# Optimization experiments

Hardware: AMD Instinct MI355X
Metric: run time of the kernel (lower is better)

## Reference

```python
import jax, jax.numpy as jnp
import numpy as np

NUM_USERS = 100000
NUM_ITEMS = 50000
N = NUM_USERS + NUM_ITEMS
EMBED_DIM = 64
NUM_LAYERS = 3
NNZ = 4800000


def setup_inputs() -> dict:
    key = jax.random.key(0)
    k1, k2, k3, k4, k5 = jax.random.split(key, 5)
    user_emb = jax.random.normal(k1, (NUM_USERS, EMBED_DIM), dtype=jnp.float32)
    item_emb = jax.random.normal(k2, (NUM_ITEMS, EMBED_DIM), dtype=jnp.float32)
    edge_src = jax.random.randint(k3, (NNZ,), 0, N, dtype=jnp.int32)
    edge_dst = jax.random.randint(k4, (NNZ,), 0, N, dtype=jnp.int32)
    edge_val = jax.random.uniform(k5, (NNZ,), dtype=jnp.float32)
    return {"user_emb": user_emb, "item_emb": item_emb,
            "edge_src": edge_src, "edge_dst": edge_dst, "edge_val": edge_val}


def _spmm(edge_src, edge_dst, edge_val, x):
    # y[src] += val * x[dst]   (COO SpMM, fixed sparsity pattern)
    msgs = edge_val[:, None] * x[edge_dst]          # [nnz, D]
    return jax.ops.segment_sum(msgs, edge_src, num_segments=N)


def reference(user_emb, item_emb, edge_src, edge_dst, edge_val):
    ego = jnp.concatenate([user_emb, item_emb], axis=0)  # [N, D]
    acc = ego  # running sum for layer-mean pooling (avoids stacking all layers)
    for _ in range(NUM_LAYERS):
        ego = _spmm(edge_src, edge_dst, edge_val, ego)
        acc = acc + ego
    out = acc / jnp.float32(NUM_LAYERS + 1)  # mean over (num_layers+1) layer embeddings
    user_final = out[:NUM_USERS]
    item_final = out[NUM_USERS:]
    return (user_final, item_final)
```

## Files before the change

### kernel.cpp

```cpp
#include <hip/hip_runtime.h>
#include <hip/hip_fp16.h>

#define NUM_USERS 100000
#define NUM_ITEMS 50000
#define NTOT (NUM_USERS + NUM_ITEMS)
#define EMBED_DIM 64
#define NNZ_E 4800000
#define NUM_LAYERS 3

#define RPB 128
#define NBUCK ((NTOT + RPB - 1) / RPB)
#define BCAP 4672
#define NSUPER 37
#define SCAP 134144
#define EPB1 4096
#define EPB2 4096
#define DMASK 0x3FFFF
#define NBIN 19
#define NKEY (RPB * NBIN)
#define NKEYP 2560

__global__ void __launch_bounds__(256)
k_init(const float* __restrict__ ue, const float* __restrict__ ie,
       __half* __restrict__ b0) {
    const long long total2 = (long long)NTOT * EMBED_DIM / 2;
    const long long u2 = (long long)NUM_USERS * EMBED_DIM / 2;
    const float2* ue2 = (const float2*)ue;
    const float2* ie2 = (const float2*)ie;
    __half2* b02 = (__half2*)b0;
    for (long long i = (long long)blockIdx.x * blockDim.x + threadIdx.x;
         i < total2; i += (long long)gridDim.x * blockDim.x) {
        float2 v = (i < u2) ? ue2[i] : ie2[i - u2];
        b02[i] = __floats2half2_rn(v.x, v.y);
    }
}

__global__ void __launch_bounds__(256)
k_super(const int* __restrict__ src, const int* __restrict__ dst,
        const float* __restrict__ val, int* __restrict__ cursorS,
        int2* __restrict__ outS) {
    __shared__ int h[NSUPER];
    __shared__ int base[NSUPER];
    __shared__ int srcbuf[EPB1];
    int t = threadIdx.x;
    if (t < NSUPER) h[t] = 0;
    __syncthreads();
    long long e0 = (long long)blockIdx.x * EPB1;
    int n = (int)(((long long)NNZ_E - e0) < EPB1 ? (NNZ_E - e0) : EPB1);
    for (int i = t; i < n; i += 256) {
        int s = __builtin_nontemporal_load(&src[e0 + i]);
        srcbuf[i] = s;
        atomicAdd(&h[s >> 12], 1);
    }
    __syncthreads();
    if (t < NSUPER) {
        int c = h[t];
        base[t] = (c > 0) ? atomicAdd(&cursorS[t], c) : 0;
        h[t] = 0;
    }
    __syncthreads();
    for (int i = t; i < n; i += 256) {
        int s = srcbuf[i];
        int d = __builtin_nontemporal_load(&dst[e0 + i]);
        float v = __builtin_nontemporal_load(&val[e0 + i]);
        int sb = s >> 12;
        int off = base[sb] + atomicAdd(&h[sb], 1);
        outS[(long long)sb * SCAP + off] =
            make_int2(d | ((s & 4095) << 18), __float_as_int(v));
    }
}

__global__ void __launch_bounds__(256)
k_bin(const int2* __restrict__ superA, const int* __restrict__ cursorS,
      int* __restrict__ cursorB, int2* __restrict__ outB) {
    __shared__ int h[32];
    __shared__ int base32[32];
    int s = blockIdx.y;
    int cnt = cursorS[s];
    int beg = blockIdx.x * EPB2;
    if (beg >= cnt) return;
    int n = (cnt - beg < EPB2) ? (cnt - beg) : EPB2;
    int t = threadIdx.x;
    const long long* in8 = (const long long*)(superA + (long long)s * SCAP + beg);
    if (t < 32) h[t] = 0;
    __syncthreads();
    for (int i = t; i < n; i += 256) {
        long long raw = __builtin_nontemporal_load(&in8[i]);
        int row12 = ((int)raw >> 18) & 4095;
        atomicAdd(&h[row12 >> 7], 1);
    }
    __syncthreads();
    if (t < 32) {
        int c = h[t];
        base32[t] = (c > 0) ? atomicAdd(&cursorB[s * 32 + t], c) : 0;
        h[t] = 0;
    }
    __syncthreads();
    for (int i = t; i < n; i += 256) {
        long long raw = __builtin_nontemporal_load(&in8[i]);
        int ex = (int)raw;
        int row12 = (ex >> 18) & 4095;
        int bl = row12 >> 7;
        int off = base32[bl] + atomicAdd(&h[bl], 1);
        outB[(long long)(s * 32 + bl) * BCAP + off] =
            make_int2((ex & DMASK) | ((row12 & 127) << 18), (int)(raw >> 32));
    }
}

__global__ void __launch_bounds__(512)
k_sortip(int2* __restrict__ buf, const int* __restrict__ cursor,
         int2* __restrict__ rp) {
    __shared__ long long stage[BCAP];
    __shared__ int h[NKEYP];
    __shared__ int part[512];
    int b = blockIdx.x;
    int t = threadIdx.x;
    int cnt = cursor[b];
    long long gb = (long long)b * BCAP;
    long long* g8 = (long long*)buf + gb;
    for (int i = t; i < NKEYP; i += 512) h[i] = 0;
    __syncthreads();
    for (int i = t; i < cnt; i += 512) {
        long long raw = __builtin_nontemporal_load(&g8[i]);
        stage[i] = raw;
        int ex = (int)raw;
        int key = ((ex >> 18) & 127) * NBIN + ((ex & DMASK) >> 13);
        atomicAdd(&h[key], 1);
    }
    __syncthreads();
    int base = t * 5;
    int l0 = h[base], l1 = h[base + 1], l2 = h[base + 2], l3 = h[base + 3],
        l4 = h[base + 4];
    int s = l0 + l1 + l2 + l3 + l4;
    part[t] = s;
    __syncthreads();
    for (int off = 1; off < 512; off <<= 1) {
        int x = (t >= off) ? part[t - off] : 0;
        __syncthreads();
        part[t] += x;
        __syncthreads();
    }
    int run = part[t] - s;
    h[base] = run;     run += l0;
    h[base + 1] = run; run += l1;
    h[base + 2] = run; run += l2;
    h[base + 3] = run; run += l3;
    h[base + 4] = run;
    __syncthreads();
    if (t < RPB) {
        int beg = h[t * NBIN];
        int end = h[(t + 1) * NBIN];
        int row = b * RPB + t;
        if (row < NTOT)
            rp[row] = make_int2((int)(gb + beg), (int)(gb + end));
    }
    __syncthreads();
    for (int i = t; i < cnt; i += 512) {
        long long raw = stage[i];
        int ex = (int)raw;
        int key = ((ex >> 18) & 127) * NBIN + ((ex & DMASK) >> 13);
        int slot = atomicAdd(&h[key], 1);
        g8[slot] = raw;
    }
}

__device__ __forceinline__ void unpack4(float2 p, float& x0, float& x1,
                                        float& x2, float& x3) {
    __half2 h01 = *(const __half2*)&p.x;
    __half2 h23 = *(const __half2*)&p.y;
    float2 f01 = __half22float2(h01);
    float2 f23 = __half22float2(h23);
    x0 = f01.x; x1 = f01.y; x2 = f23.x; x3 = f23.y;
}

template <int U>
__device__ __forceinline__ void gg(const int2* __restrict__ edges, int j, int grp,
                                   int l16, const float2* __restrict__ xq,
                                   float& a0, float& a1, float& a2, float& a3) {
    int2 e[U];
    float2 xv[U];
#pragma unroll
    for (int k = 0; k < U; ++k) e[k] = edges[j + grp * U + k];
#pragma unroll
    for (int k = 0; k < U; ++k)
        xv[k] = xq[(long long)(e[k].x & DMASK) * 16 + l16];
#pragma unroll
    for (int k = 0; k < U; ++k) {
        float w = __int_as_float(e[k].y);
        float x0, x1, x2, x3;
        unpack4(xv[k], x0, x1, x2, x3);
        a0 = fmaf(w, x0, a0);
        a1 = fmaf(w, x1, a1);
        a2 = fmaf(w, x2, a2);
        a3 = fmaf(w, x3, a3);
    }
}

template <bool LAST>
__global__ void __launch_bounds__(256)
k_spmm_csr(const int2* __restrict__ edges, const int2* __restrict__ rp,
           const __half* __restrict__ x, __half* __restrict__ nxt,
           const __half* __restrict__ eb0, const __half* __restrict__ eb1,
           float* __restrict__ out) {
    int row = blockIdx.x * 4 + (threadIdx.x >> 6);
    int lane = threadIdx.x & 63;
    if (row >= NTOT) return;
    int2 be = rp[row];
    int beg = be.x;
    int end = be.y;
    int grp = lane >> 4;
    int l16 = lane & 15;
    const float2* xq = (const float2*)x;
    float a0 = 0.f, a1 = 0.f, a2 = 0.f, a3 = 0.f;
    int j = beg;
    for (; j + 32 <= end; j += 32) gg<8>(edges, j, grp, l16, xq, a0, a1, a2, a3);
    if (j + 16 <= end) { gg<4>(edges, j, grp, l16, xq, a0, a1, a2, a3); j += 16; }
    if (j + 8 <= end)  { gg<2>(edges, j, grp, l16, xq, a0, a1, a2, a3); j += 8; }
    for (int t2 = j + grp; t2 < end; t2 += 4) {
        int2 e = edges[t2];
        float w = __int_as_float(e.y);
        float x0, x1, x2, x3;
        unpack4(xq[(long long)(e.x & DMASK) * 16 + l16], x0, x1, x2, x3);
        a0 = fmaf(w, x0, a0);
        a1 = fmaf(w, x1, a1);
        a2 = fmaf(w, x2, a2);
        a3 = fmaf(w, x3, a3);
    }
    a0 += __shfl_xor(a0, 16); a1 += __shfl_xor(a1, 16);
    a2 += __shfl_xor(a2, 16); a3 += __shfl_xor(a3, 16);
    a0 += __shfl_xor(a0, 32); a1 += __shfl_xor(a1, 32);
    a2 += __shfl_xor(a2, 32); a3 += __shfl_xor(a3, 32);
    if (grp == 0) {
        if (!LAST) {
            union { __half2 h[2]; float2 f; } u;
            u.h[0] = __floats2half2_rn(a0, a1);
            u.h[1] = __floats2half2_rn(a2, a3);
            ((float2*)nxt)[(long long)row * 16 + l16] = u.f;
        } else {
            float v0, v1, v2, v3, w0, w1, w2, w3, z0, z1, z2, z3;
            unpack4(((const float2*)eb0)[(long long)row * 16 + l16], v0, v1, v2, v3);
            unpack4(((const float2*)eb1)[(long long)row * 16 + l16], w0, w1, w2, w3);
            unpack4(xq[(long long)row * 16 + l16], z0, z1, z2, z3);
            const float s = 1.0f / (NUM_LAYERS + 1);
            float4 r;
            r.x = (v0 + w0 + z0 + a0) * s;
            r.y = (v1 + w1 + z1 + a1) * s;
            r.z = (v2 + w2 + z2 + a2) * s;
            r.w = (v3 + w3 + z3 + a3) * s;
            ((float4*)out)[(long long)row * 16 + l16] = r;
        }
    }
}

extern "C" void kernel_launch(void* const* d_in, const int* in_sizes, int n_in,
                              void* d_out, int out_size, void* d_ws, size_t ws_size,
                              hipStream_t stream) {
    const float* user_emb = (const float*)d_in[0];
    const float* item_emb = (const float*)d_in[1];
    const int* edge_src   = (const int*)d_in[2];
    const int* edge_dst   = (const int*)d_in[3];
    const float* edge_val = (const float*)d_in[4];
    float* out = (float*)d_out;

    auto al = [](size_t x) { return (x + 255) & ~(size_t)255; };
    const size_t halfMat   = (size_t)NTOT * EMBED_DIM * sizeof(__half);
    const size_t buckBytes = al((size_t)NBUCK * BCAP * sizeof(int2));
    const size_t rpBytes   = al(((size_t)NTOT + 8) * sizeof(int2));

    char* p = (char*)d_ws;
    __half* b0 = (__half*)p;
    __half* b1 = (__half*)(p + halfMat);
    __half* b2 = (__half*)(p + 2 * halfMat);
    int2* superA = (int2*)d_ws;
    p += 3 * halfMat;
    int2* bucketedB = (int2*)p;          p += buckBytes;
    int2* rp = (int2*)p;                 p += rpBytes;
    int* cursorS = (int*)p;
    int* cursorB = cursorS + 64;

    hipMemsetAsync(cursorS, 0, 8192, stream);

    hipLaunchKernelGGL(k_super, dim3((NNZ_E + EPB1 - 1) / EPB1), dim3(256), 0,
                       stream, edge_src, edge_dst, edge_val, cursorS, superA);
    hipLaunchKernelGGL(k_bin, dim3((SCAP + EPB2 - 1) / EPB2, NSUPER), dim3(256),
                       0, stream, superA, cursorS, cursorB, bucketedB);
    hipLaunchKernelGGL(k_sortip, dim3(NBUCK), dim3(512), 0, stream,
                       bucketedB, cursorB, rp);
    hipLaunchKernelGGL(k_init, dim3(2048), dim3(256), 0, stream,
                       user_emb, item_emb, b0);

    const int spmmBlocks = (NTOT + 3) / 4;
    hipLaunchKernelGGL((k_spmm_csr<false>), dim3(spmmBlocks), dim3(256), 0,
                       stream, bucketedB, rp, b0, b1,
                       (const __half*)nullptr, (const __half*)nullptr, out);
    hipLaunchKernelGGL((k_spmm_csr<false>), dim3(spmmBlocks), dim3(256), 0,
                       stream, bucketedB, rp, b1, b2,
                       (const __half*)nullptr, (const __half*)nullptr, out);
    hipLaunchKernelGGL((k_spmm_csr<true>), dim3(spmmBlocks), dim3(256), 0,
                       stream, bucketedB, rp, b2, (__half*)nullptr,
                       b0, b1, out);
}
```

Before: 411.7 us.

## Replace per-row CSR SpMM with column-binned segmented SpMM over buckets

The sort kernel now keys edges by row and by one of 10 coarse column bins, and stores a per-row table of bin offsets instead of a single begin/end pair. The new SpMM kernel gives each 32-lane group 8 consecutive rows and walks the column bins in order, so all groups in a block gather from the same slice of the embedding matrix at the same time. The aim is better L2 reuse of the gathered half-precision rows. In exchange it gives up the old unrolled multi-edge gathers, leaving a short, serial per-row loop with little memory-level parallelism and fewer, larger blocks.

```diff
diff --git a/kernel.cpp b/kernel.cpp
--- a/kernel.cpp
+++ b/kernel.cpp
@@ -16,9 +16,9 @@
 #define EPB1 4096
 #define EPB2 4096
 #define DMASK 0x3FFFF
-#define NBIN 19
+#define NBIN 10
 #define NKEY (RPB * NBIN)
-#define NKEYP 2560
+#define RPS 16
 
 __global__ void __launch_bounds__(256)
 k_init(const float* __restrict__ ue, const float* __restrict__ ie,
@@ -109,145 +109,121 @@
 
 __global__ void __launch_bounds__(512)
 k_sortip(int2* __restrict__ buf, const int* __restrict__ cursor,
-         int2* __restrict__ rp) {
+         int* __restrict__ rp16) {
     __shared__ long long stage[BCAP];
-    __shared__ int h[NKEYP];
-    __shared__ int part[512];
+    __shared__ int h[NKEY];
+    __shared__ int part[256];
     int b = blockIdx.x;
     int t = threadIdx.x;
     int cnt = cursor[b];
     long long gb = (long long)b * BCAP;
     long long* g8 = (long long*)buf + gb;
-    for (int i = t; i < NKEYP; i += 512) h[i] = 0;
+    for (int i = t; i < NKEY; i += 512) h[i] = 0;
     __syncthreads();
     for (int i = t; i < cnt; i += 512) {
         long long raw = __builtin_nontemporal_load(&g8[i]);
         stage[i] = raw;
         int ex = (int)raw;
-        int key = ((ex >> 18) & 127) * NBIN + ((ex & DMASK) >> 13);
+        int key = ((ex >> 18) & 127) * NBIN + ((ex & DMASK) >> 14);
         atomicAdd(&h[key], 1);
     }
     __syncthreads();
+    int l0 = 0, l1 = 0, l2 = 0, l3 = 0, l4 = 0, s = 0;
     int base = t * 5;
-    int l0 = h[base], l1 = h[base + 1], l2 = h[base + 2], l3 = h[base + 3],
-        l4 = h[base + 4];
-    int s = l0 + l1 + l2 + l3 + l4;
-    part[t] = s;
-    __syncthreads();
-    for (int off = 1; off < 512; off <<= 1) {
-        int x = (t >= off) ? part[t - off] : 0;
+    if (t < 256) {
+        l0 = h[base]; l1 = h[base + 1]; l2 = h[base + 2];
+        l3 = h[base + 3]; l4 = h[base + 4];
+        s = l0 + l1 + l2 + l3 + l4;
+        part[t] = s;
+    }
+    __syncthreads();
+    for (int off = 1; off < 256; off <<= 1) {
+        int x = 0;
+        if (t < 256 && t >= off) x = part[t - off];
         __syncthreads();
-        part[t] += x;
+        if (t < 256) part[t] += x;
         __syncthreads();
     }
-    int run = part[t] - s;
-    h[base] = run;     run += l0;
-    h[base + 1] = run; run += l1;
-    h[base + 2] = run; run += l2;
-    h[base + 3] = run; run += l3;
-    h[base + 4] = run;
+    if (t < 256) {
+        int run = part[t] - s;
+        h[base] = run;     run += l0;
+        h[base + 1] = run; run += l1;
+        h[base + 2] = run; run += l2;
+        h[base + 3] = run; run += l3;
+        h[base + 4] = run;
+    }
     __syncthreads();
     if (t < RPB) {
-        int beg = h[t * NBIN];
-        int end = h[(t + 1) * NBIN];
         int row = b * RPB + t;
-        if (row < NTOT)
-            rp[row] = make_int2((int)(gb + beg), (int)(gb + end));
+        int gbi = (int)gb;
+#pragma unroll
+        for (int q = 0; q < NBIN; ++q)
+            rp16[row * RPS + q] = gbi + h[t * NBIN + q];
+        int end = (t == RPB - 1) ? cnt : h[(t + 1) * NBIN];
+        rp16[row * RPS + NBIN] = gbi + end;
     }
     __syncthreads();
     for (int i = t; i < cnt; i += 512) {
         long long raw = stage[i];
         int ex = (int)raw;
-        int key = ((ex >> 18) & 127) * NBIN + ((ex & DMASK) >> 13);
+        int key = ((ex >> 18) & 127) * NBIN + ((ex & DMASK) >> 14);
         int slot = atomicAdd(&h[key], 1);
         g8[slot] = raw;
     }
 }
 
-__device__ __forceinline__ void unpack4(float2 p, float& x0, float& x1,
-                                        float& x2, float& x3) {
-    __half2 h01 = *(const __half2*)&p.x;
-    __half2 h23 = *(const __half2*)&p.y;
-    float2 f01 = __half22float2(h01);
-    float2 f23 = __half22float2(h23);
-    x0 = f01.x; x1 = f01.y; x2 = f23.x; x3 = f23.y;
-}
-
-template <int U>
-__device__ __forceinline__ void gg(const int2* __restrict__ edges, int j, int grp,
-                                   int l16, const float2* __restrict__ xq,
-                                   float& a0, float& a1, float& a2, float& a3) {
-    int2 e[U];
-    float2 xv[U];
-#pragma unroll
-    for (int k = 0; k < U; ++k) e[k] = edges[j + grp * U + k];
-#pragma unroll
-    for (int k = 0; k < U; ++k)
-        xv[k] = xq[(long long)(e[k].x & DMASK) * 16 + l16];
-#pragma unroll
-    for (int k = 0; k < U; ++k) {
-        float w = __int_as_float(e[k].y);
-        float x0, x1, x2, x3;
-        unpack4(xv[k], x0, x1, x2, x3);
-        a0 = fmaf(w, x0, a0);
-        a1 = fmaf(w, x1, a1);
-        a2 = fmaf(w, x2, a2);
-        a3 = fmaf(w, x3, a3);
-    }
-}
-
 template <bool LAST>
-__global__ void __launch_bounds__(256)
-k_spmm_csr(const int2* __restrict__ edges, const int2* __restrict__ rp,
+__global__ void __launch_bounds__(512)
+k_spmm_seg(const int2* __restrict__ edges, const int* __restrict__ rp16,
            const __half* __restrict__ x, __half* __restrict__ nxt,
            const __half* __restrict__ eb0, const __half* __restrict__ eb1,
            float* __restrict__ out) {
-    int row = blockIdx.x * 4 + (threadIdx.x >> 6);
-    int lane = threadIdx.x & 63;
-    if (row >= NTOT) return;
-    int2 be = rp[row];
-    int beg = be.x;
-    int end = be.y;
-    int grp = lane >> 4;
-    int l16 = lane & 15;
-    const float2* xq = (const float2*)x;
-    float a0 = 0.f, a1 = 0.f, a2 = 0.f, a3 = 0.f;
-    int j = beg;
-    for (; j + 32 <= end; j += 32) gg<8>(edges, j, grp, l16, xq, a0, a1, a2, a3);
-    if (j + 16 <= end) { gg<4>(edges, j, grp, l16, xq, a0, a1, a2, a3); j += 16; }
-    if (j + 8 <= end)  { gg<2>(edges, j, grp, l16, xq, a0, a1, a2, a3); j += 8; }
-    for (int t2 = j + grp; t2 < end; t2 += 4) {
-        int2 e = edges[t2];
-        float w = __int_as_float(e.y);
-        float x0, x1, x2, x3;
-        unpack4(xq[(long long)(e.x & DMASK) * 16 + l16], x0, x1, x2, x3);
-        a0 = fmaf(w, x0, a0);
-        a1 = fmaf(w, x1, a1);
-        a2 = fmaf(w, x2, a2);
-        a3 = fmaf(w, x3, a3);
-    }
-    a0 += __shfl_xor(a0, 16); a1 += __shfl_xor(a1, 16);
-    a2 += __shfl_xor(a2, 16); a3 += __shfl_xor(a3, 16);
-    a0 += __shfl_xor(a0, 32); a1 += __shfl_xor(a1, 32);
-    a2 += __shfl_xor(a2, 32); a3 += __shfl_xor(a3, 32);
-    if (grp == 0) {
-        if (!LAST) {
-            union { __half2 h[2]; float2 f; } u;
-            u.h[0] = __floats2half2_rn(a0, a1);
-            u.h[1] = __floats2half2_rn(a2, a3);
-            ((float2*)nxt)[(long long)row * 16 + l16] = u.f;
-        } else {
-            float v0, v1, v2, v3, w0, w1, w2, w3, z0, z1, z2, z3;
-            unpack4(((const float2*)eb0)[(long long)row * 16 + l16], v0, v1, v2, v3);
-            unpack4(((const float2*)eb1)[(long long)row * 16 + l16], w0, w1, w2, w3);
-            unpack4(xq[(long long)row * 16 + l16], z0, z1, z2, z3);
-            const float s = 1.0f / (NUM_LAYERS + 1);
-            float4 r;
-            r.x = (v0 + w0 + z0 + a0) * s;
-            r.y = (v1 + w1 + z1 + a1) * s;
-            r.z = (v2 + w2 + z2 + a2) * s;
-            r.w = (v3 + w3 + z3 + a3) * s;
-            ((float4*)out)[(long long)row * 16 + l16] = r;
+    int t = threadIdx.x;
+    int gidx = t >> 5;
+    int l32 = t & 31;
+    const __half2* x2 = (const __half2*)x;
+    const long long* e8 = (const long long*)edges;
+
+    for (int half = 0; half < 2; ++half) {
+        int bucket = blockIdx.x * 2 + half;
+        int row0 = bucket * RPB + gidx * 8;
+        float2 acc[8];
+#pragma unroll
+        for (int r = 0; r < 8; ++r) acc[r] = make_float2(0.f, 0.f);
+
+        for (int s = 0; s < NBIN; ++s) {
+#pragma unroll
+            for (int r = 0; r < 8; ++r) {
+                int row = row0 + r;
+                int jb = rp16[row * RPS + s];
+                int je = rp16[row * RPS + s + 1];
+                for (int j = jb; j < je; ++j) {
+                    long long raw = e8[j];
+                    float w = __int_as_float((int)(raw >> 32));
+                    __half2 xv = x2[(long long)((int)raw & DMASK) * 32 + l32];
+                    float2 xf = __half22float2(xv);
+                    acc[r].x = fmaf(w, xf.x, acc[r].x);
+                    acc[r].y = fmaf(w, xf.y, acc[r].y);
+                }
+            }
+        }
+#pragma unroll
+        for (int r = 0; r < 8; ++r) {
+            int row = row0 + r;
+            if (row >= NTOT) continue;
+            if (!LAST) {
+                ((__half2*)nxt)[(long long)row * 32 + l32] =
+                    __floats2half2_rn(acc[r].x, acc[r].y);
+            } else {
+                float2 v = __half22float2(((const __half2*)eb0)[(long long)row * 32 + l32]);
+                float2 a = __half22float2(((const __half2*)eb1)[(long long)row * 32 + l32]);
+                float2 z = __half22float2(x2[(long long)row * 32 + l32]);
+                const float sc = 1.0f / (NUM_LAYERS + 1);
+                float2 rr;
+                rr.x = (v.x + a.x + z.x + acc[r].x) * sc;
+                rr.y = (v.y + a.y + z.y + acc[r].y) * sc;
+                ((float2*)out)[(long long)row * 32 + l32] = rr;
+            }
         }
     }
 }
@@ -265,7 +241,7 @@
     auto al = [](size_t x) { return (x + 255) & ~(size_t)255; };
     const size_t halfMat   = (size_t)NTOT * EMBED_DIM * sizeof(__half);
     const size_t buckBytes = al((size_t)NBUCK * BCAP * sizeof(int2));
-    const size_t rpBytes   = al(((size_t)NTOT + 8) * sizeof(int2));
+    const size_t rpBytes   = al((size_t)NBUCK * RPB * RPS * sizeof(int));
 
     char* p = (char*)d_ws;
     __half* b0 = (__half*)p;
@@ -274,7 +250,7 @@
     int2* superA = (int2*)d_ws;
     p += 3 * halfMat;
     int2* bucketedB = (int2*)p;          p += buckBytes;
-    int2* rp = (int2*)p;                 p += rpBytes;
+    int* rp16 = (int*)p;                 p += rpBytes;
     int* cursorS = (int*)p;
     int* cursorB = cursorS + 64;
 
@@ -285,18 +261,18 @@
     hipLaunchKernelGGL(k_bin, dim3((SCAP + EPB2 - 1) / EPB2, NSUPER), dim3(256),
                        0, stream, superA, cursorS, cursorB, bucketedB);
     hipLaunchKernelGGL(k_sortip, dim3(NBUCK), dim3(512), 0, stream,
-                       bucketedB, cursorB, rp);
+                       bucketedB, cursorB, rp16);
     hipLaunchKernelGGL(k_init, dim3(2048), dim3(256), 0, stream,
                        user_emb, item_emb, b0);
 
-    const int spmmBlocks = (NTOT + 3) / 4;
-    hipLaunchKernelGGL((k_spmm_csr<false>), dim3(spmmBlocks), dim3(256), 0,
-                       stream, bucketedB, rp, b0, b1,
+    const int segBlocks = NBUCK / 2;
+    hipLaunchKernelGGL((k_spmm_seg<false>), dim3(segBlocks), dim3(512), 0,
+                       stream, bucketedB, rp16, b0, b1,
                        (const __half*)nullptr, (const __half*)nullptr, out);
-    hipLaunchKernelGGL((k_spmm_csr<false>), dim3(spmmBlocks), dim3(256), 0,
-                       stream, bucketedB, rp, b1, b2,
+    hipLaunchKernelGGL((k_spmm_seg<false>), dim3(segBlocks), dim3(512), 0,
+                       stream, bucketedB, rp16, b1, b2,
                        (const __half*)nullptr, (const __half*)nullptr, out);
-    hipLaunchKernelGGL((k_spmm_csr<true>), dim3(spmmBlocks), dim3(256), 0,
-                       stream, bucketedB, rp, b2, (__half*)nullptr,
+    hipLaunchKernelGGL((k_spmm_seg<true>), dim3(segBlocks), dim3(512), 0,
+                       stream, bucketedB, rp16, b2, (__half*)nullptr,
                        b0, b1, out);
 }
```

After: 1.500 ms. +264.4%, slower.
